# Kernel tuning notes

Measured on AMD Instinct MI355X. Metric: run time of the kernel, lower is better.

## Reference

```python
import jax, jax.numpy as jnp
import numpy as np

N_NODES = 100000
N_EDGES = 1600000
NEG_SLOPE = 0.2  # PyG GATConv default
BN_EPS = 1e-5


def gat_conv(x, src, dst, W, a_src, a_dst, bias):
    # x: [N, F], W: [F, H, C]
    h = jnp.einsum('nf,fhc->nhc', x, W)                 # [N, H, C]
    al_src = jnp.sum(h * a_src, axis=-1)                # [N, H]
    al_dst = jnp.sum(h * a_dst, axis=-1)                # [N, H]
    e = al_src[src] + al_dst[dst]                       # [E, H]
    e = jnp.where(e >= 0, e, NEG_SLOPE * e)             # leaky_relu(0.2)
    # segment softmax over incoming edges of each dst node
    emax = jax.ops.segment_max(e, dst, num_segments=N_NODES)
    ee = jnp.exp(e - emax[dst])
    denom = jax.ops.segment_sum(ee, dst, num_segments=N_NODES)
    alpha = ee / denom[dst]                             # [E, H]
    msg = alpha[:, :, None] * h[src]                    # [E, H, C]
    out = jax.ops.segment_sum(msg, dst, num_segments=N_NODES)  # [N, H, C]
    return out.mean(axis=1) + bias                      # concat=False -> head mean


def batch_norm(x, gamma, beta):
    mu = jnp.mean(x, axis=0)
    var = jnp.var(x, axis=0)  # biased, as in torch BN normalization
    return (x - mu) * jax.lax.rsqrt(var + BN_EPS) * gamma + beta


def setup_inputs() -> dict:
    key = jax.random.key(0)
    ks = jax.random.split(key, 16)
    inp = {
        'x': jax.random.normal(ks[0], (N_NODES, 128), jnp.float32),
        'edge_index': jax.random.randint(ks[1], (2, N_EDGES), 0, N_NODES, jnp.int64)
            if jax.config.jax_enable_x64 else
            jax.random.randint(ks[1], (2, N_EDGES), 0, N_NODES, jnp.int32),
        'edge_attr': jax.random.normal(ks[2], (N_EDGES, 8), jnp.float32),
        'W0': 0.1 * jax.random.normal(ks[3], (128, 4, 32), jnp.float32),
        'a_src0': 0.1 * jax.random.normal(ks[4], (4, 32), jnp.float32),
        'a_dst0': 0.1 * jax.random.normal(ks[5], (4, 32), jnp.float32),
        'b0': jnp.zeros((32,), jnp.float32),
        'g0': jnp.ones((32,), jnp.float32),
        'be0': jnp.zeros((32,), jnp.float32),
        'W1': 0.1 * jax.random.normal(ks[6], (32, 4, 32), jnp.float32),
        'a_src1': 0.1 * jax.random.normal(ks[7], (4, 32), jnp.float32),
        'a_dst1': 0.1 * jax.random.normal(ks[8], (4, 32), jnp.float32),
        'b1': jnp.zeros((32,), jnp.float32),
        'g1': jnp.ones((32,), jnp.float32),
        'be1': jnp.zeros((32,), jnp.float32),
        'W2': 0.1 * jax.random.normal(ks[9], (32, 4, 32), jnp.float32),
        'a_src2': 0.1 * jax.random.normal(ks[10], (4, 32), jnp.float32),
        'a_dst2': 0.1 * jax.random.normal(ks[11], (4, 32), jnp.float32),
        'b2': jnp.zeros((32,), jnp.float32),
    }
    return inp


def reference(x, edge_index, edge_attr, W0, a_src0, a_dst0, b0, g0, be0,
              W1, a_src1, a_dst1, b1, g1, be1, W2, a_src2, a_dst2, b2):
    src, dst = edge_index[0], edge_index[1]
    h = gat_conv(x, src, dst, W0, a_src0, a_dst0, b0)
    h = jax.nn.relu(batch_norm(h, g0, be0))  # dropout = identity (deterministic ref)
    h = gat_conv(h, src, dst, W1, a_src1, a_dst1, b1)
    h = jax.nn.relu(batch_norm(h, g1, be1))
    h = gat_conv(h, src, dst, W2, a_src2, a_dst2, b2)
    return (h, edge_attr)
```

## Files before the change

### kernel.cpp

```cpp
#include <hip/hip_runtime.h>
#include <cstdio>
#include <cstdint>

#define LRELU 0.2f
#define BN_EPS 1e-5f

typedef short bf16x8 __attribute__((ext_vector_type(8)));
typedef float f32x4 __attribute__((ext_vector_type(4)));

__device__ inline unsigned short f2bf(float f) {
  unsigned int u = __float_as_uint(f);
  u += 0x7fffu + ((u >> 16) & 1u);
  return (unsigned short)(u >> 16);
}
__device__ inline float bf2f(unsigned short v) {
  return __uint_as_float(((unsigned int)v) << 16);
}


__global__ __launch_bounds__(256) void k_deg_bhist(const int* __restrict__ dst,
                                                   int* __restrict__ deg,
                                                   int* __restrict__ bh, int E) {
  __shared__ int cnt[512];
  for (int b = threadIdx.x; b < 512; b += 256) cnt[b] = 0;
  __syncthreads();
  for (int i = blockIdx.x * blockDim.x + threadIdx.x; i < E;
       i += gridDim.x * blockDim.x) {
    int d = dst[i];
    atomicAdd(&deg[d], 1);
    atomicAdd(&cnt[d >> 8], 1);
  }
  __syncthreads();
  for (int b = threadIdx.x; b < 512; b += 256)
    if (cnt[b]) atomicAdd(&bh[b], cnt[b]);
}

__global__ void k_scan_tile(const int* __restrict__ deg, int* __restrict__ offs,
                            int* __restrict__ tilesum, int N) {
  __shared__ int sh[256];
  int i = blockIdx.x * 256 + threadIdx.x;
  int v = (i < N) ? deg[i] : 0;
  sh[threadIdx.x] = v;
  __syncthreads();
  for (int s = 1; s < 256; s <<= 1) {
    int t = (threadIdx.x >= s) ? sh[threadIdx.x - s] : 0;
    __syncthreads();
    sh[threadIdx.x] += t;
    __syncthreads();
  }
  if (i < N) offs[i] = sh[threadIdx.x] - v;
  if (threadIdx.x == 255) tilesum[blockIdx.x] = sh[255];
}

__global__ __launch_bounds__(512) void k_exscan2(
    const int* __restrict__ tilesum, int* __restrict__ tilepre,
    const int* __restrict__ bh, int* __restrict__ bstart,
    int* __restrict__ bcur, int n, int* __restrict__ etot) {
  __shared__ int sh[512];
  const int t = threadIdx.x;
  int v = (t < n) ? tilesum[t] : 0;
  sh[t] = v;
  __syncthreads();
  for (int s = 1; s < 512; s <<= 1) {
    int u = (t >= s) ? sh[t - s] : 0;
    __syncthreads();
    sh[t] += u;
    __syncthreads();
  }
  if (t < n) tilepre[t] = sh[t] - v;
  if (t == n - 1) *etot = sh[t];
  __syncthreads();
  int v2 = (t < n) ? bh[t] : 0;
  sh[t] = v2;
  __syncthreads();
  for (int s = 1; s < 512; s <<= 1) {
    int u = (t >= s) ? sh[t - s] : 0;
    __syncthreads();
    sh[t] += u;
    __syncthreads();
  }
  if (t < n) {
    int ex = sh[t] - v2;
    bstart[t] = ex;
    bcur[t] = ex;
  }
  if (t == n - 1) bstart[n] = sh[t];
}

__global__ void k_addfix(int* __restrict__ offs, const int* __restrict__ tilepre,
                         int N) {
  int i = blockIdx.x * blockDim.x + threadIdx.x;
  if (i < N) offs[i] += tilepre[i >> 8];
}

__global__ __launch_bounds__(256) void k_bscatter(const int* __restrict__ src,
                                                  const int* __restrict__ dst,
                                                  int* __restrict__ bcur,
                                                  uint2* __restrict__ bpair, int E) {
  __shared__ int cnt[512];
  const int chunk = (E + gridDim.x - 1) / gridDim.x;
  const int beg = blockIdx.x * chunk;
  const int end = min(E, beg + chunk);
  for (int b = threadIdx.x; b < 512; b += 256) cnt[b] = 0;
  __syncthreads();
  for (int e = beg + threadIdx.x; e < end; e += 256)
    atomicAdd(&cnt[dst[e] >> 8], 1);
  __syncthreads();
  for (int b = threadIdx.x; b < 512; b += 256) {
    int c = cnt[b];
    cnt[b] = (c > 0) ? atomicAdd(&bcur[b], c) : 0;
  }
  __syncthreads();
  for (int e = beg + threadIdx.x; e < end; e += 256) {
    int d = dst[e];
    int pos = atomicAdd(&cnt[d >> 8], 1);
    bpair[pos] = make_uint2((unsigned)src[e], (unsigned)d);
  }
}

__global__ __launch_bounds__(256) void k_bcsr(const uint2* __restrict__ bpair,
                                              const int* __restrict__ bstart,
                                              const int* __restrict__ offs,
                                              int* __restrict__ srcs, int N) {
  __shared__ int cur[256];
  const int b = blockIdx.x;
  const int lo = b << 8;
  if (lo + (int)threadIdx.x < N) cur[threadIdx.x] = offs[lo + threadIdx.x];
  __syncthreads();
  const int e0 = bstart[b], e1 = bstart[b + 1];
  for (int e = e0 + threadIdx.x; e < e1; e += 256) {
    uint2 p = bpair[e];
    int pos = atomicAdd(&cur[p.y & 255], 1);
    srcs[pos] = (int)p.x;
  }
}

__global__ void k_castW3(const float* __restrict__ W0, const float* __restrict__ W1,
                         const float* __restrict__ W2,
                         unsigned short* __restrict__ Wt0,
                         unsigned short* __restrict__ Wt1,
                         unsigned short* __restrict__ Wt2) {
  int o = blockIdx.x * 256 + threadIdx.x;
  if (o < 16384) {
    int n = o >> 7, k = o & 127;
    Wt0[o] = f2bf(W0[k * 128 + n]);
  } else if (o < 20480) {
    int p = o - 16384, n = p >> 5, k = p & 31;
    Wt1[p] = f2bf(W1[k * 128 + n]);
  } else if (o < 24576) {
    int p = o - 20480, n = p >> 5, k = p & 31;
    Wt2[p] = f2bf(W2[k * 128 + n]);
  }
}

template <int K, bool BN>
__global__ __launch_bounds__(256) void k_mfma(
    const float* __restrict__ Ain, const unsigned short* __restrict__ Wt,
    const float* __restrict__ asrc, const float* __restrict__ adst,
    const float* __restrict__ stats, const float* __restrict__ g,
    const float* __restrict__ be,
    unsigned short* __restrict__ h, float* __restrict__ als,
    float* __restrict__ ald, int N) {
  __shared__ unsigned short lsh[4][16 * 132];
  __shared__ float sc_s[32], sh_s[32];
  const int wv   = threadIdx.x >> 6;
  const int lane = threadIdx.x & 63;
  const int quad = lane >> 4;
  const int col  = lane & 15;
  const int m0   = blockIdx.x * 64 + wv * 16;
  const int rowc = min(m0 + col, N - 1);

  if constexpr (BN) {
    if (threadIdx.x < 32) {
      float s = 0.f, ss = 0.f;
#pragma unroll
      for (int r = 0; r < 8; r++) {
        s  += stats[r * 64 + threadIdx.x];
        ss += stats[r * 64 + 32 + threadIdx.x];
      }
      const float inv = 1.f / (float)N;
      const float mu = s * inv;
      const float var = ss * inv - mu * mu;
      const float scv = g[threadIdx.x] * rsqrtf(var + BN_EPS);
      sc_s[threadIdx.x] = scv;
      sh_s[threadIdx.x] = be[threadIdx.x] - mu * scv;
    }
    __syncthreads();
  }

  f32x4 acc[8];
#pragma unroll
  for (int t = 0; t < 8; t++) acc[t] = (f32x4){0.f, 0.f, 0.f, 0.f};

#pragma unroll
  for (int ks = 0; ks < K / 32; ks++) {
    const int k0 = ks * 32 + quad * 8;
    const float* ap = Ain + (size_t)rowc * K + k0;
    float4 f0 = *(const float4*)ap;
    float4 f1 = *(const float4*)(ap + 4);
    bf16x8 a;
    if constexpr (BN) {
      f0.x = fmaxf(0.f, fmaf(f0.x, sc_s[k0 + 0], sh_s[k0 + 0]));
      f0.y = fmaxf(0.f, fmaf(f0.y, sc_s[k0 + 1], sh_s[k0 + 1]));
      f0.z = fmaxf(0.f, fmaf(f0.z, sc_s[k0 + 2], sh_s[k0 + 2]));
      f0.w = fmaxf(0.f, fmaf(f0.w, sc_s[k0 + 3], sh_s[k0 + 3]));
      f1.x = fmaxf(0.f, fmaf(f1.x, sc_s[k0 + 4], sh_s[k0 + 4]));
      f1.y = fmaxf(0.f, fmaf(f1.y, sc_s[k0 + 5], sh_s[k0 + 5]));
      f1.z = fmaxf(0.f, fmaf(f1.z, sc_s[k0 + 6], sh_s[k0 + 6]));
      f1.w = fmaxf(0.f, fmaf(f1.w, sc_s[k0 + 7], sh_s[k0 + 7]));
    }
    a[0] = (short)f2bf(f0.x); a[1] = (short)f2bf(f0.y);
    a[2] = (short)f2bf(f0.z); a[3] = (short)f2bf(f0.w);
    a[4] = (short)f2bf(f1.x); a[5] = (short)f2bf(f1.y);
    a[6] = (short)f2bf(f1.z); a[7] = (short)f2bf(f1.w);
#pragma unroll
    for (int t = 0; t < 8; t++) {
      bf16x8 b = *(const bf16x8*)(Wt + (size_t)(t * 16 + col) * K + k0);
      acc[t] = __builtin_amdgcn_mfma_f32_16x16x32_bf16(a, b, acc[t], 0, 0, 0);
    }
  }

#pragma unroll
  for (int t = 0; t < 8; t++) {
#pragma unroll
    for (int j = 0; j < 4; j++)
      lsh[wv][(quad * 4 + j) * 132 + col + 16 * t] = f2bf(acc[t][j]);
  }
  __syncthreads();

  float as8[8], ad8[8];
#pragma unroll
  for (int j = 0; j < 8; j++) {
    as8[j] = asrc[col * 8 + j];
    ad8[j] = adst[col * 8 + j];
  }

#pragma unroll
  for (int i = 0; i < 4; i++) {
    const int row = i * 4 + quad;
    const int hrow = m0 + row;
    const unsigned short* rp = &lsh[wv][row * 132 + col * 8];
    ushort4 lo = *(const ushort4*)rp;
    ushort4 hi = *(const ushort4*)(rp + 4);
    float p = 0.f, q = 0.f, v;
    v = bf2f(lo.x); p += v * as8[0]; q += v * ad8[0];
    v = bf2f(lo.y); p += v * as8[1]; q += v * ad8[1];
    v = bf2f(lo.z); p += v * as8[2]; q += v * ad8[2];
    v = bf2f(lo.w); p += v * as8[3]; q += v * ad8[3];
    v = bf2f(hi.x); p += v * as8[4]; q += v * ad8[4];
    v = bf2f(hi.y); p += v * as8[5]; q += v * ad8[5];
    v = bf2f(hi.z); p += v * as8[6]; q += v * ad8[6];
    v = bf2f(hi.w); p += v * as8[7]; q += v * ad8[7];
    if (hrow < N) {
      ushort4* gp = (ushort4*)(h + (size_t)hrow * 128 + col * 8);
      gp[0] = lo; gp[1] = hi;
    }
    p += __shfl_xor(p, 1); p += __shfl_xor(p, 2);
    q += __shfl_xor(q, 1); q += __shfl_xor(q, 2);
    if ((lane & 3) == 0 && hrow < N) {
      const int head = col >> 2;
      als[hrow * 4 + head] = p;
      ald[hrow * 4 + head] = q;
    }
  }
}

template <bool STATS>
__global__ __launch_bounds__(256) void k_agg(
    const unsigned int* __restrict__ h2, const float* __restrict__ als,
    const float* __restrict__ ald, const int* __restrict__ offs,
    const int* __restrict__ srcs, const float* __restrict__ bias,
    float* __restrict__ y, float* __restrict__ stats, int N) {
  __shared__ float s1[32], s2[32];
  const int node = blockIdx.x * 4 + (threadIdx.x >> 6);
  const int lane = threadIdx.x & 63;
  const bool valid = node < N;
  if constexpr (STATS) {
    if (threadIdx.x < 32) { s1[threadIdx.x] = 0.f; s2[threadIdx.x] = 0.f; }
    __syncthreads();
  } else {
    if (!valid) return;
  }

  float outx = 0.f, outy = 0.f;
  if (valid) {
    const int head = lane >> 4;
    const int beg = __builtin_amdgcn_readfirstlane(offs[node]);
    const int end = __builtin_amdgcn_readfirstlane(offs[node + 1]);
    const float ad = ald[node * 4 + head];
    float ax = 0.f, ay = 0.f, dn = 0.f;

    for (int base = beg; base < end; base += 64) {
      const int m = min(64, end - base);
      const int sv = srcs[base + min(lane, m - 1)];
      int j = 0;
      for (; j + 4 <= m; j += 4) {
        const int s0 = __builtin_amdgcn_readlane(sv, j + 0);
        const int s1r = __builtin_amdgcn_readlane(sv, j + 1);
        const int s2r = __builtin_amdgcn_readlane(sv, j + 2);
        const int s3 = __builtin_amdgcn_readlane(sv, j + 3);
        const float a0 = als[s0 * 4 + head];
        const float a1 = als[s1r * 4 + head];
        const float a2 = als[s2r * 4 + head];
        const float a3 = als[s3 * 4 + head];
        const unsigned int u0 = h2[(size_t)s0 * 64 + lane];
        const unsigned int u1 = h2[(size_t)s1r * 64 + lane];
        const unsigned int u2 = h2[(size_t)s2r * 64 + lane];
        const unsigned int u3 = h2[(size_t)s3 * 64 + lane];
        float e0 = a0 + ad; e0 = fmaxf(e0, LRELU * e0);
        float e1 = a1 + ad; e1 = fmaxf(e1, LRELU * e1);
        float e2 = a2 + ad; e2 = fmaxf(e2, LRELU * e2);
        float e3 = a3 + ad; e3 = fmaxf(e3, LRELU * e3);
        const float w0 = __expf(e0), w1 = __expf(e1);
        const float w2 = __expf(e2), w3 = __expf(e3);
        dn += w0 + w1 + w2 + w3;
        ax = fmaf(w0, __uint_as_float(u0 << 16), ax);
        ay = fmaf(w0, __uint_as_float(u0 & 0xffff0000u), ay);
        ax = fmaf(w1, __uint_as_float(u1 << 16), ax);
        ay = fmaf(w1, __uint_as_float(u1 & 0xffff0000u), ay);
        ax = fmaf(w2, __uint_as_float(u2 << 16), ax);
        ay = fmaf(w2, __uint_as_float(u2 & 0xffff0000u), ay);
        ax = fmaf(w3, __uint_as_float(u3 << 16), ax);
        ay = fmaf(w3, __uint_as_float(u3 & 0xffff0000u), ay);
      }
      for (; j < m; j++) {
        const int s = __builtin_amdgcn_readlane(sv, j);
        const float a = als[s * 4 + head];
        const unsigned int u = h2[(size_t)s * 64 + lane];
        float ev = a + ad;
        ev = fmaxf(ev, LRELU * ev);
        const float w = __expf(ev);
        dn += w;
        ax = fmaf(w, __uint_as_float(u << 16), ax);
        ay = fmaf(w, __uint_as_float(u & 0xffff0000u), ay);
      }
    }

    const float r = (dn > 0.f) ? (1.f / dn) : 0.f;
    ax *= r; ay *= r;
    ax += __shfl_xor(ax, 16); ay += __shfl_xor(ay, 16);
    ax += __shfl_xor(ax, 32); ay += __shfl_xor(ay, 32);
    if (lane < 16) {
      float2 b2 = ((const float2*)bias)[lane];
      float2 o;
      o.x = 0.25f * ax + b2.x;
      o.y = 0.25f * ay + b2.y;
      ((float2*)(y + (size_t)node * 32))[lane] = o;
      outx = o.x; outy = o.y;
    }
  }

  if constexpr (STATS) {
    if (valid && lane < 16) {
      atomicAdd(&s1[2 * lane], outx);
      atomicAdd(&s1[2 * lane + 1], outy);
      atomicAdd(&s2[2 * lane], outx * outx);
      atomicAdd(&s2[2 * lane + 1], outy * outy);
    }
    __syncthreads();
    if (threadIdx.x < 32) {
      float* sb = stats + (blockIdx.x & 7) * 64;
      atomicAdd(&sb[threadIdx.x], s1[threadIdx.x]);
      atomicAdd(&sb[32 + threadIdx.x], s2[threadIdx.x]);
    }
  }
}

__global__ void k_copy4(const float4* __restrict__ s, float4* __restrict__ d, int n) {
  int i = blockIdx.x * blockDim.x + threadIdx.x;
  if (i < n) d[i] = s[i];
}

extern "C" void kernel_launch(void* const* d_in, const int* in_sizes, int n_in,
                              void* d_out, int out_size, void* d_ws, size_t ws_size,
                              hipStream_t stream) {
  const float* x   = (const float*)d_in[0];
  const int*   ei  = (const int*)d_in[1];
  const float* ea  = (const float*)d_in[2];
  const float* W0  = (const float*)d_in[3];
  const float* as0 = (const float*)d_in[4];
  const float* ad0 = (const float*)d_in[5];
  const float* b0  = (const float*)d_in[6];
  const float* g0  = (const float*)d_in[7];
  const float* be0 = (const float*)d_in[8];
  const float* W1  = (const float*)d_in[9];
  const float* as1 = (const float*)d_in[10];
  const float* ad1 = (const float*)d_in[11];
  const float* b1  = (const float*)d_in[12];
  const float* g1  = (const float*)d_in[13];
  const float* be1 = (const float*)d_in[14];
  const float* W2  = (const float*)d_in[15];
  const float* as2 = (const float*)d_in[16];
  const float* ad2 = (const float*)d_in[17];
  const float* b2  = (const float*)d_in[18];

  const int N = in_sizes[0] / 128;
  const int E = in_sizes[1] / 2;
  const int* srcI = ei;
  const int* dstI = ei + E;
  const int NB = (N + 255) >> 8;
  const int nb = NB;

  char* w = (char*)d_ws;
  auto carve = [&](size_t bytes) -> void* {
    void* p = (void*)w;
    w += (bytes + 255) & ~(size_t)255;
    return p;
  };
  unsigned short* h  = (unsigned short*)carve((size_t)N * 128 * 2);
  float* als        = (float*)carve((size_t)N * 4 * 4);
  float* ald        = (float*)carve((size_t)N * 4 * 4);
  float* y          = (float*)carve((size_t)N * 32 * 4);
  int* offs         = (int*)carve((size_t)(N + 1) * 4);
  int* srcs         = (int*)carve((size_t)E * 4);
  int* deg          = (int*)carve((size_t)N * 4);
  int* bh           = (int*)carve(512 * 4);
  float* stats      = (float*)carve(1024 * 4);
  char* zend        = w;
  int* tilesum      = (int*)carve((size_t)nb * 4);
  int* tilepre      = (int*)carve((size_t)nb * 4);
  int* bstart       = (int*)carve(513 * 4);
  int* bcur         = (int*)carve(512 * 4);
  unsigned short* Wt0 = (unsigned short*)carve(128 * 128 * 2);
  unsigned short* Wt1 = (unsigned short*)carve(128 * 32 * 2);
  unsigned short* Wt2 = (unsigned short*)carve(128 * 32 * 2);
  if ((size_t)(w - (char*)d_ws) > ws_size) {
    fprintf(stderr, "GAT kernel: ws too small (%zu needed, %zu given)\n",
            (size_t)(w - (char*)d_ws), ws_size);
    return;
  }
  uint2* bpair = (uint2*)h;

  hipMemsetAsync(deg, 0, (size_t)(zend - (char*)deg), stream);

  k_deg_bhist<<<256, 256, 0, stream>>>(dstI, deg, bh, E);
  k_scan_tile<<<nb, 256, 0, stream>>>(deg, offs, tilesum, N);
  k_exscan2<<<1, 512, 0, stream>>>(tilesum, tilepre, bh, bstart, bcur, nb, offs + N);
  k_addfix<<<(N + 255) / 256, 256, 0, stream>>>(offs, tilepre, N);
  k_bscatter<<<128, 256, 0, stream>>>(srcI, dstI, bcur, bpair, E);
  k_bcsr<<<NB, 256, 0, stream>>>(bpair, bstart, offs, srcs, N);

  k_castW3<<<96, 256, 0, stream>>>(W0, W1, W2, Wt0, Wt1, Wt2);

  const int gGemm = (N + 63) / 64;
  const int gAgg  = (N + 3) / 4;
  float* out_nodes = (float*)d_out;
  float* out_ea    = out_nodes + (size_t)N * 32;

  k_mfma<128, false><<<gGemm, 256, 0, stream>>>(x, Wt0, as0, ad0,
                                                nullptr, nullptr, nullptr,
                                                h, als, ald, N);
  k_agg<true><<<gAgg, 256, 0, stream>>>((const unsigned int*)h, als, ald, offs,
                                        srcs, b0, y, stats, N);
  k_mfma<32, true><<<gGemm, 256, 0, stream>>>(y, Wt1, as1, ad1, stats, g0, be0,
                                              h, als, ald, N);
  k_agg<true><<<gAgg, 256, 0, stream>>>((const unsigned int*)h, als, ald, offs,
                                        srcs, b1, y, stats + 512, N);
  k_mfma<32, true><<<gGemm, 256, 0, stream>>>(y, Wt2, as2, ad2, stats + 512, g1, be1,
                                              h, als, ald, N);
  k_agg<false><<<gAgg, 256, 0, stream>>>((const unsigned int*)h, als, ald, offs,
                                         srcs, b2, out_nodes, nullptr, N);
  const int n4 = E * 2;
  k_copy4<<<(n4 + 255) / 256, 256, 0, stream>>>((const float4*)ea, (float4*)out_ea, n4);
}
```

Baseline: 667.2 us.

## Compute CSR offsets per bucket, fuse edge_attr copy, pair edges in aggregation

The global per-node degree atomics and the three-kernel scan (tile scan, block prefix, fixup) are removed. Each bucket block in the CSR build now counts its own per-node degrees in shared memory and scans them locally to produce offsets. The edge_attr copy is folded into the histogram kernel, which cuts launches. The aggregation kernel now handles two edges per wavefront, one per half-wave, with 8-byte loads of four bf16 channels, then reduces the halves with shuffles. This gives more memory-level parallelism per gather at the cost of extra shuffle reductions and wasted work on odd-edge tails.

```diff
diff --git a/kernel.cpp b/kernel.cpp
--- a/kernel.cpp
+++ b/kernel.cpp
@@ -16,49 +16,35 @@
 __device__ inline float bf2f(unsigned short v) {
   return __uint_as_float(((unsigned int)v) << 16);
 }
-
-
-__global__ __launch_bounds__(256) void k_deg_bhist(const int* __restrict__ dst,
-                                                   int* __restrict__ deg,
-                                                   int* __restrict__ bh, int E) {
+__device__ inline float bflo(unsigned int u) { return __uint_as_float(u << 16); }
+__device__ inline float bfhi(unsigned int u) { return __uint_as_float(u & 0xffff0000u); }
+
+
+__global__ __launch_bounds__(256) void k_bhist_copy(const int* __restrict__ dst,
+                                                    int* __restrict__ bh,
+                                                    const float4* __restrict__ ea,
+                                                    float4* __restrict__ oea,
+                                                    int E) {
   __shared__ int cnt[512];
   for (int b = threadIdx.x; b < 512; b += 256) cnt[b] = 0;
   __syncthreads();
-  for (int i = blockIdx.x * blockDim.x + threadIdx.x; i < E;
-       i += gridDim.x * blockDim.x) {
-    int d = dst[i];
-    atomicAdd(&deg[d], 1);
-    atomicAdd(&cnt[d >> 8], 1);
-  }
+  const int gid = blockIdx.x * blockDim.x + threadIdx.x;
+  const int gstride = gridDim.x * blockDim.x;
+  for (int i = gid; i < E; i += gstride) atomicAdd(&cnt[dst[i] >> 8], 1);
+  const int n4 = E * 2;
+  for (int i = gid; i < n4; i += gstride) oea[i] = ea[i];
   __syncthreads();
   for (int b = threadIdx.x; b < 512; b += 256)
     if (cnt[b]) atomicAdd(&bh[b], cnt[b]);
 }
 
-__global__ void k_scan_tile(const int* __restrict__ deg, int* __restrict__ offs,
-                            int* __restrict__ tilesum, int N) {
-  __shared__ int sh[256];
-  int i = blockIdx.x * 256 + threadIdx.x;
-  int v = (i < N) ? deg[i] : 0;
-  sh[threadIdx.x] = v;
-  __syncthreads();
-  for (int s = 1; s < 256; s <<= 1) {
-    int t = (threadIdx.x >= s) ? sh[threadIdx.x - s] : 0;
-    __syncthreads();
-    sh[threadIdx.x] += t;
-    __syncthreads();
-  }
-  if (i < N) offs[i] = sh[threadIdx.x] - v;
-  if (threadIdx.x == 255) tilesum[blockIdx.x] = sh[255];
-}
-
-__global__ __launch_bounds__(512) void k_exscan2(
-    const int* __restrict__ tilesum, int* __restrict__ tilepre,
-    const int* __restrict__ bh, int* __restrict__ bstart,
-    int* __restrict__ bcur, int n, int* __restrict__ etot) {
+__global__ __launch_bounds__(512) void k_exscan(const int* __restrict__ bh,
+                                                int* __restrict__ bstart,
+                                                int* __restrict__ bcur, int n,
+                                                int* __restrict__ offsN) {
   __shared__ int sh[512];
   const int t = threadIdx.x;
-  int v = (t < n) ? tilesum[t] : 0;
+  int v = (t < n) ? bh[t] : 0;
   sh[t] = v;
   __syncthreads();
   for (int s = 1; s < 512; s <<= 1) {
@@ -67,30 +53,15 @@
     sh[t] += u;
     __syncthreads();
   }
-  if (t < n) tilepre[t] = sh[t] - v;
-  if (t == n - 1) *etot = sh[t];
-  __syncthreads();
-  int v2 = (t < n) ? bh[t] : 0;
-  sh[t] = v2;
-  __syncthreads();
-  for (int s = 1; s < 512; s <<= 1) {
-    int u = (t >= s) ? sh[t - s] : 0;
-    __syncthreads();
-    sh[t] += u;
-    __syncthreads();
-  }
   if (t < n) {
-    int ex = sh[t] - v2;
+    int ex = sh[t] - v;
     bstart[t] = ex;
     bcur[t] = ex;
   }
-  if (t == n - 1) bstart[n] = sh[t];
-}
-
-__global__ void k_addfix(int* __restrict__ offs, const int* __restrict__ tilepre,
-                         int N) {
-  int i = blockIdx.x * blockDim.x + threadIdx.x;
-  if (i < N) offs[i] += tilepre[i >> 8];
+  if (t == n - 1) {
+    bstart[n] = sh[t];
+    *offsN = sh[t];
+  }
 }
 
 __global__ __launch_bounds__(256) void k_bscatter(const int* __restrict__ src,
@@ -118,17 +89,32 @@
   }
 }
 
-__global__ __launch_bounds__(256) void k_bcsr(const uint2* __restrict__ bpair,
-                                              const int* __restrict__ bstart,
-                                              const int* __restrict__ offs,
-                                              int* __restrict__ srcs, int N) {
+__global__ __launch_bounds__(256) void k_bcsr2(const uint2* __restrict__ bpair,
+                                               const int* __restrict__ bstart,
+                                               int* __restrict__ offs,
+                                               int* __restrict__ srcs, int N) {
+  __shared__ int sc[256];
   __shared__ int cur[256];
   const int b = blockIdx.x;
   const int lo = b << 8;
-  if (lo + (int)threadIdx.x < N) cur[threadIdx.x] = offs[lo + threadIdx.x];
-  __syncthreads();
+  const int t = threadIdx.x;
   const int e0 = bstart[b], e1 = bstart[b + 1];
-  for (int e = e0 + threadIdx.x; e < e1; e += 256) {
+  sc[t] = 0;
+  __syncthreads();
+  for (int e = e0 + t; e < e1; e += 256) atomicAdd(&sc[bpair[e].y & 255], 1);
+  __syncthreads();
+  int v = sc[t];
+  for (int s = 1; s < 256; s <<= 1) {
+    int u = (t >= s) ? sc[t - s] : 0;
+    __syncthreads();
+    sc[t] += u;
+    __syncthreads();
+  }
+  const int pos0 = e0 + sc[t] - v;
+  cur[t] = pos0;
+  if (lo + t < N) offs[lo + t] = pos0;
+  __syncthreads();
+  for (int e = e0 + t; e < e1; e += 256) {
     uint2 p = bpair[e];
     int pos = atomicAdd(&cur[p.y & 255], 1);
     srcs[pos] = (int)p.x;
@@ -282,81 +268,85 @@
     if (!valid) return;
   }
 
-  float outx = 0.f, outy = 0.f;
   if (valid) {
-    const int head = lane >> 4;
+    const int half = lane >> 5;
+    const int sub  = lane & 31;
+    const int head = sub >> 3;
     const int beg = __builtin_amdgcn_readfirstlane(offs[node]);
     const int end = __builtin_amdgcn_readfirstlane(offs[node + 1]);
     const float ad = ald[node * 4 + head];
-    float ax = 0.f, ay = 0.f, dn = 0.f;
+    float ax0 = 0.f, ax1 = 0.f, ax2 = 0.f, ax3 = 0.f, dn = 0.f;
 
     for (int base = beg; base < end; base += 64) {
       const int m = min(64, end - base);
       const int sv = srcs[base + min(lane, m - 1)];
       int j = 0;
-      for (; j + 4 <= m; j += 4) {
-        const int s0 = __builtin_amdgcn_readlane(sv, j + 0);
-        const int s1r = __builtin_amdgcn_readlane(sv, j + 1);
-        const int s2r = __builtin_amdgcn_readlane(sv, j + 2);
-        const int s3 = __builtin_amdgcn_readlane(sv, j + 3);
-        const float a0 = als[s0 * 4 + head];
-        const float a1 = als[s1r * 4 + head];
-        const float a2 = als[s2r * 4 + head];
-        const float a3 = als[s3 * 4 + head];
-        const unsigned int u0 = h2[(size_t)s0 * 64 + lane];
-        const unsigned int u1 = h2[(size_t)s1r * 64 + lane];
-        const unsigned int u2 = h2[(size_t)s2r * 64 + lane];
-        const unsigned int u3 = h2[(size_t)s3 * 64 + lane];
-        float e0 = a0 + ad; e0 = fmaxf(e0, LRELU * e0);
-        float e1 = a1 + ad; e1 = fmaxf(e1, LRELU * e1);
-        float e2 = a2 + ad; e2 = fmaxf(e2, LRELU * e2);
-        float e3 = a3 + ad; e3 = fmaxf(e3, LRELU * e3);
-        const float w0 = __expf(e0), w1 = __expf(e1);
-        const float w2 = __expf(e2), w3 = __expf(e3);
-        dn += w0 + w1 + w2 + w3;
-        ax = fmaf(w0, __uint_as_float(u0 << 16), ax);
-        ay = fmaf(w0, __uint_as_float(u0 & 0xffff0000u), ay);
-        ax = fmaf(w1, __uint_as_float(u1 << 16), ax);
-        ay = fmaf(w1, __uint_as_float(u1 & 0xffff0000u), ay);
-        ax = fmaf(w2, __uint_as_float(u2 << 16), ax);
-        ay = fmaf(w2, __uint_as_float(u2 & 0xffff0000u), ay);
-        ax = fmaf(w3, __uint_as_float(u3 << 16), ax);
-        ay = fmaf(w3, __uint_as_float(u3 & 0xffff0000u), ay);
+
+#define PAIR(J)                                                            \
+  {                                                                        \
+    const int sA = __builtin_amdgcn_readlane(sv, (J));                     \
+    const int sB = __builtin_amdgcn_readlane(sv, (J) + 1);                 \
+    const int s = half ? sB : sA;                                          \
+    const float a = als[s * 4 + head];                                     \
+    const uint2 u = *(const uint2*)(h2 + (size_t)s * 64 + (sub << 1));     \
+    float e = a + ad;                                                      \
+    e = fmaxf(e, LRELU * e);                                               \
+    const float w = __expf(e);                                             \
+    dn += w;                                                               \
+    ax0 = fmaf(w, bflo(u.x), ax0);                                         \
+    ax1 = fmaf(w, bfhi(u.x), ax1);                                         \
+    ax2 = fmaf(w, bflo(u.y), ax2);                                         \
+    ax3 = fmaf(w, bfhi(u.y), ax3);                                         \
+  }
+
+      for (; j + 8 <= m; j += 8) {
+        PAIR(j) PAIR(j + 2) PAIR(j + 4) PAIR(j + 6)
       }
-      for (; j < m; j++) {
+      for (; j + 2 <= m; j += 2) { PAIR(j) }
+      if (j < m) {
         const int s = __builtin_amdgcn_readlane(sv, j);
         const float a = als[s * 4 + head];
-        const unsigned int u = h2[(size_t)s * 64 + lane];
-        float ev = a + ad;
-        ev = fmaxf(ev, LRELU * ev);
-        const float w = __expf(ev);
+        const uint2 u = *(const uint2*)(h2 + (size_t)s * 64 + (sub << 1));
+        float e = a + ad;
+        e = fmaxf(e, LRELU * e);
+        const float w = half ? 0.f : __expf(e);
         dn += w;
-        ax = fmaf(w, __uint_as_float(u << 16), ax);
-        ay = fmaf(w, __uint_as_float(u & 0xffff0000u), ay);
+        ax0 = fmaf(w, bflo(u.x), ax0);
+        ax1 = fmaf(w, bfhi(u.x), ax1);
+        ax2 = fmaf(w, bflo(u.y), ax2);
+        ax3 = fmaf(w, bfhi(u.y), ax3);
       }
-    }
-
+#undef PAIR
+    }
+
+    dn += __shfl_xor(dn, 32);
     const float r = (dn > 0.f) ? (1.f / dn) : 0.f;
-    ax *= r; ay *= r;
-    ax += __shfl_xor(ax, 16); ay += __shfl_xor(ay, 16);
-    ax += __shfl_xor(ax, 32); ay += __shfl_xor(ay, 32);
-    if (lane < 16) {
-      float2 b2 = ((const float2*)bias)[lane];
-      float2 o;
-      o.x = 0.25f * ax + b2.x;
-      o.y = 0.25f * ay + b2.y;
-      ((float2*)(y + (size_t)node * 32))[lane] = o;
-      outx = o.x; outy = o.y;
+    ax0 *= r; ax1 *= r; ax2 *= r; ax3 *= r;
+    ax0 += __shfl_xor(ax0, 32); ax1 += __shfl_xor(ax1, 32);
+    ax2 += __shfl_xor(ax2, 32); ax3 += __shfl_xor(ax3, 32);
+    ax0 += __shfl_xor(ax0, 8);  ax1 += __shfl_xor(ax1, 8);
+    ax2 += __shfl_xor(ax2, 8);  ax3 += __shfl_xor(ax3, 8);
+    ax0 += __shfl_xor(ax0, 16); ax1 += __shfl_xor(ax1, 16);
+    ax2 += __shfl_xor(ax2, 16); ax3 += __shfl_xor(ax3, 16);
+
+    if (lane < 8) {
+      float4 b4 = ((const float4*)bias)[lane];
+      float4 o;
+      o.x = 0.25f * ax0 + b4.x;
+      o.y = 0.25f * ax1 + b4.y;
+      o.z = 0.25f * ax2 + b4.z;
+      o.w = 0.25f * ax3 + b4.w;
+      ((float4*)(y + (size_t)node * 32))[lane] = o;
+      if constexpr (STATS) {
+        atomicAdd(&s1[4 * lane + 0], o.x); atomicAdd(&s2[4 * lane + 0], o.x * o.x);
+        atomicAdd(&s1[4 * lane + 1], o.y); atomicAdd(&s2[4 * lane + 1], o.y * o.y);
+        atomicAdd(&s1[4 * lane + 2], o.z); atomicAdd(&s2[4 * lane + 2], o.z * o.z);
+        atomicAdd(&s1[4 * lane + 3], o.w); atomicAdd(&s2[4 * lane + 3], o.w * o.w);
+      }
     }
   }
 
   if constexpr (STATS) {
-    if (valid && lane < 16) {
-      atomicAdd(&s1[2 * lane], outx);
-      atomicAdd(&s1[2 * lane + 1], outy);
-      atomicAdd(&s2[2 * lane], outx * outx);
-      atomicAdd(&s2[2 * lane + 1], outy * outy);
-    }
     __syncthreads();
     if (threadIdx.x < 32) {
       float* sb = stats + (blockIdx.x & 7) * 64;
@@ -364,11 +354,6 @@
       atomicAdd(&sb[32 + threadIdx.x], s2[threadIdx.x]);
     }
   }
-}
-
-__global__ void k_copy4(const float4* __restrict__ s, float4* __restrict__ d, int n) {
-  int i = blockIdx.x * blockDim.x + threadIdx.x;
-  if (i < n) d[i] = s[i];
 }
 
 extern "C" void kernel_launch(void* const* d_in, const int* in_sizes, int n_in,
@@ -399,7 +384,6 @@
   const int* srcI = ei;
   const int* dstI = ei + E;
   const int NB = (N + 255) >> 8;
-  const int nb = NB;
 
   char* w = (char*)d_ws;
   auto carve = [&](size_t bytes) -> void* {
@@ -413,12 +397,9 @@
   float* y          = (float*)carve((size_t)N * 32 * 4);
   int* offs         = (int*)carve((size_t)(N + 1) * 4);
   int* srcs         = (int*)carve((size_t)E * 4);
-  int* deg          = (int*)carve((size_t)N * 4);
   int* bh           = (int*)carve(512 * 4);
   float* stats      = (float*)carve(1024 * 4);
   char* zend        = w;
-  int* tilesum      = (int*)carve((size_t)nb * 4);
-  int* tilepre      = (int*)carve((size_t)nb * 4);
   int* bstart       = (int*)carve(513 * 4);
   int* bcur         = (int*)carve(512 * 4);
   unsigned short* Wt0 = (unsigned short*)carve(128 * 128 * 2);
@@ -431,21 +412,21 @@
   }
   uint2* bpair = (uint2*)h;
 
-  hipMemsetAsync(deg, 0, (size_t)(zend - (char*)deg), stream);
-
-  k_deg_bhist<<<256, 256, 0, stream>>>(dstI, deg, bh, E);
-  k_scan_tile<<<nb, 256, 0, stream>>>(deg, offs, tilesum, N);
-  k_exscan2<<<1, 512, 0, stream>>>(tilesum, tilepre, bh, bstart, bcur, nb, offs + N);
-  k_addfix<<<(N + 255) / 256, 256, 0, stream>>>(offs, tilepre, N);
+  float* out_nodes = (float*)d_out;
+  float* out_ea    = out_nodes + (size_t)N * 32;
+
+  hipMemsetAsync(bh, 0, (size_t)(zend - (char*)bh), stream);
+
+  k_bhist_copy<<<256, 256, 0, stream>>>(dstI, bh, (const float4*)ea,
+                                        (float4*)out_ea, E);
+  k_exscan<<<1, 512, 0, stream>>>(bh, bstart, bcur, NB, offs + N);
   k_bscatter<<<128, 256, 0, stream>>>(srcI, dstI, bcur, bpair, E);
-  k_bcsr<<<NB, 256, 0, stream>>>(bpair, bstart, offs, srcs, N);
+  k_bcsr2<<<NB, 256, 0, stream>>>(bpair, bstart, offs, srcs, N);
 
   k_castW3<<<96, 256, 0, stream>>>(W0, W1, W2, Wt0, Wt1, Wt2);
 
   const int gGemm = (N + 63) / 64;
   const int gAgg  = (N + 3) / 4;
-  float* out_nodes = (float*)d_out;
-  float* out_ea    = out_nodes + (size_t)N * 32;
 
   k_mfma<128, false><<<gGemm, 256, 0, stream>>>(x, Wt0, as0, ad0,
                                                 nullptr, nullptr, nullptr,
@@ -460,6 +441,4 @@
                                               h, als, ald, N);
   k_agg<false><<<gAgg, 256, 0, stream>>>((const unsigned int*)h, als, ald, offs,
                                          srcs, b2, out_nodes, nullptr, N);
-  const int n4 = E * 2;
-  k_copy4<<<(n4 + 255) / 256, 256, 0, stream>>>((const float4*)ea, (float4*)out_ea, n4);
-}
+}
```

Result: faster. 615.9 us (-7.7%).
